# Kernel tuning notes

Hardware: AMD Instinct MI355X
Metric: run time of the kernel (lower is better)

## Reference

```python
import jax, jax.numpy as jnp
import numpy as np
import math

B, N, CS, CZ, H, HD, PQ, PV = 1, 512, 1024, 128, 12, 16, 4, 8
INF, EPS = 1e5, 1e-8


def _quat_to_rot(q):
    q = q / jnp.linalg.norm(q, axis=-1, keepdims=True)
    w, x, y, z = q[..., 0], q[..., 1], q[..., 2], q[..., 3]
    R = jnp.stack([
        1 - 2 * (y * y + z * z), 2 * (x * y - w * z), 2 * (x * z + w * y),
        2 * (x * y + w * z), 1 - 2 * (x * x + z * z), 2 * (y * z - w * x),
        2 * (x * z - w * y), 2 * (y * z + w * x), 1 - 2 * (x * x + y * y)
    ], axis=-1)
    return R.reshape(q.shape[:-1] + (3, 3))


def _split3(x):
    # torch.split into 3 chunks along last dim, then stack on new last dim
    d = x.shape[-1] // 3
    return jnp.stack((x[..., :d], x[..., d:2 * d], x[..., 2 * d:]), axis=-1)


def setup_inputs():
    key = jax.random.key(0)
    ks = jax.random.split(key, 12)

    def lin(k, din, dout):
        kw, kb = jax.random.split(k)
        W = jax.random.normal(kw, (din, dout), jnp.float32) / np.float32(np.sqrt(din))
        b = jax.random.normal(kb, (dout,), jnp.float32) * 0.01
        return W, b

    s = jax.random.normal(ks[0], (B, N, CS), jnp.float32)
    z = jax.random.normal(ks[1], (B, N, N, CZ), jnp.float32)
    rot = _quat_to_rot(jax.random.normal(ks[2], (B, N, 4), jnp.float32))
    trans = jax.random.normal(ks[3], (B, N, 3), jnp.float32) * 10.0
    mask = jnp.ones((B, N), jnp.float32)

    Wq, bq = lin(ks[4], CS, H * HD)
    Wkv, bkv = lin(ks[5], CS, 2 * H * HD)
    Wqp, bqp = lin(ks[6], CS, H * PQ * 3)
    Wkvp, bkvp = lin(ks[7], CS, H * (PQ + PV) * 3)
    Wb, bb = lin(ks[8], CZ, H)
    head_w = jax.random.normal(ks[9], (H,), jnp.float32) * 0.5
    Wout, bout = lin(ks[10], H * (CZ + HD + PV * 4), CS)

    return dict(s=s, z=z, rot=rot, trans=trans, mask=mask,
                Wq=Wq, bq=bq, Wkv=Wkv, bkv=bkv, Wqp=Wqp, bqp=bqp,
                Wkvp=Wkvp, bkvp=bkvp, Wb=Wb, bb=bb, head_w=head_w,
                Wout=Wout, bout=bout)


def _ipa(s, z, rot, trans, mask, Wq, bq, Wkv, bkv, Wqp, bqp, Wkvp, bkvp, Wb, bb, head_w, Wout, bout):
    # scalar q, k, v : [B, N, H, HD]
    q = (s @ Wq + bq).reshape(B, N, H, HD)
    kv = (s @ Wkv + bkv).reshape(B, N, H, 2 * HD)
    k, v = kv[..., :HD], kv[..., HD:]

    # point q/k/v in global frame: p' = R p + t
    q_pts = _split3(s @ Wqp + bqp)                      # [B, N, H*PQ, 3]
    q_pts = jnp.einsum('bnij,bnpj->bnpi', rot, q_pts) + trans[:, :, None, :]
    q_pts = q_pts.reshape(B, N, H, PQ, 3)

    kv_pts = _split3(s @ Wkvp + bkvp)                   # [B, N, H*(PQ+PV), 3]
    kv_pts = jnp.einsum('bnij,bnpj->bnpi', rot, kv_pts) + trans[:, :, None, :]
    kv_pts = kv_pts.reshape(B, N, H, PQ + PV, 3)
    k_pts, v_pts = kv_pts[..., :PQ, :], kv_pts[..., PQ:, :]

    # pair bias [B, N, N, H]
    b = z @ Wb + bb

    # scalar attention logits [B, H, N, N]
    a = jnp.einsum('bihd,bjhd->bhij', q, k) * np.float32(math.sqrt(1.0 / (3 * HD)))
    a = a + np.float32(math.sqrt(1.0 / 3)) * jnp.transpose(b, (0, 3, 1, 2))

    # point-distance attention: [B, N, N, H, PQ]
    diff = q_pts[:, :, None] - k_pts[:, None]           # [B, N, N, H, PQ, 3]
    pt_att = jnp.sum(diff * diff, axis=-1)
    hw = jax.nn.softplus(head_w) * np.float32(math.sqrt(1.0 / (3 * (PQ * 9.0 / 2))))
    pt_att = jnp.sum(pt_att * hw[:, None], axis=-1) * (-0.5)   # [B, N, N, H]
    a = a + jnp.transpose(pt_att, (0, 3, 1, 2))

    square_mask = INF * (mask[:, :, None] * mask[:, None, :] - 1.0)  # [B, N, N]
    a = jax.nn.softmax(a + square_mask[:, None], axis=-1)            # [B, H, N, N]

    # scalar output [B, N, H*HD]
    o = jnp.einsum('bhij,bjhd->bihd', a, v).reshape(B, N, H * HD)

    # point output, back to local frame: R^T (p - t)
    o_pt = jnp.einsum('bhij,bjhpc->bihpc', a, v_pts)                 # [B, N, H, PV, 3]
    o_pt = jnp.einsum('bnji,bnhpj->bnhpi', rot, o_pt - trans[:, :, None, None, :])
    o_pt_norm = jnp.sqrt(jnp.sum(o_pt * o_pt, axis=-1) + EPS).reshape(B, N, H * PV)
    o_pt_r = o_pt.reshape(B, N, H * PV, 3)

    # pair output [B, N, H*CZ]
    o_pair = jnp.einsum('bhij,bijc->bihc', a, z).reshape(B, N, H * CZ)

    cat = jnp.concatenate(
        (o, o_pt_r[..., 0], o_pt_r[..., 1], o_pt_r[..., 2], o_pt_norm, o_pair), axis=-1)
    return cat @ Wout + bout


def reference(s, z, rot, trans, mask, Wq, bq, Wkv, bkv, Wqp, bqp, Wkvp, bkvp, Wb, bb, head_w, Wout, bout):
    return _ipa(s, z, rot, trans, mask, Wq, bq, Wkv, bkv, Wqp, bqp, Wkvp, bkvp, Wb, bb, head_w, Wout, bout)
```

## Files before the change

kernel.cpp:

```cpp
#include <hip/hip_runtime.h>
#include <hip/hip_bf16.h>

#define N 512
#define CS 1024
#define CZ 128
#define H 12
#define HD 16

__device__ int sniff_f32(const unsigned short* p) {
    int bad = 0;
    for (int i = 0; i < 32; ++i) {
        unsigned short u = p[i];
        int e = (u >> 7) & 0xFF;
        if (e == 0xFF || e >= 141 || (e <= 27 && (u & 0x7FFFu) != 0)) bad++;
    }
    return bad > 0;
}

__device__ __forceinline__ float ld(const void* p, int i, int f32) {
    return f32 ? ((const float*)p)[i]
               : __bfloat162float(((const __hip_bfloat16*)p)[i]);
}

__device__ __forceinline__ float bfu(unsigned short u) {
    return __bfloat162float(*(const __hip_bfloat16*)&u);
}

typedef __attribute__((ext_vector_type(8))) short bf16x8;
typedef __attribute__((ext_vector_type(4))) float f32x4;
typedef __attribute__((ext_vector_type(4))) unsigned short u16x4;
typedef __attribute__((ext_vector_type(8))) unsigned short u16x8;

#define FG_LDA 40

__device__ __forceinline__ unsigned int split_bf16(float x) {
    __hip_bfloat16 hb = __float2bfloat16(x);
    float hf = __bfloat162float(hb);
    __hip_bfloat16 lb = __float2bfloat16(x - hf);
    unsigned int h = *reinterpret_cast<unsigned short*>(&hb);
    unsigned int l = *reinterpret_cast<unsigned short*>(&lb);
    return h | (l << 16);
}

__device__ __forceinline__ void wcat_resolve(int col,
        const void* Wq, const void* Wkv, const void* Wqp, const void* Wkvp,
        const void*& W, int& cc, int& ldim) {
    if (col < 192)      { W = Wq;   cc = col;       ldim = 192; }
    else if (col < 576) { W = Wkv;  cc = col - 192; ldim = 384; }
    else if (col < 720) { W = Wqp;  cc = col - 576; ldim = 144; }
    else                { W = Wkvp; cc = col - 720; ldim = 432; }
}

__global__ void proj_gemm(const void* s,
                          const void* Wq, const void* Wkv,
                          const void* Wqp, const void* Wkvp,
                          float* rawP)
{
    __shared__ unsigned short Ah[32][FG_LDA], Al[32][FG_LDA];
    __shared__ unsigned short Bh[64][FG_LDA], Bl[64][FG_LDA];
    __shared__ int flag;
    int t = threadIdx.x;
    int bn = blockIdx.x;
    int bm = blockIdx.y;
    if (t == 0) flag = sniff_f32((const unsigned short*)s);
    __syncthreads();
    int f32 = flag;

    int w  = t >> 6, l = t & 63;
    int wm = w >> 1, wn = w & 1;
    int lr = l & 15, lq = l >> 4;

    int am = t >> 3, aq = t & 7;
    int bc = t >> 2, bq = t & 3;

    const void* Wsrc; int wcc, wld;
    wcat_resolve(bn * 64 + bc, Wq, Wkv, Wqp, Wkvp, Wsrc, wcc, wld);

    f32x4 acc0 = {0.f, 0.f, 0.f, 0.f};
    f32x4 acc1 = {0.f, 0.f, 0.f, 0.f};

    int arowbase = (bm * 32 + am) * CS;

    for (int kt = 0; kt < CS / 32; ++kt) {
        {
            int base = arowbase + kt * 32 + aq * 4;
            u16x4 hh, ll;
            #pragma unroll
            for (int e = 0; e < 4; ++e) {
                unsigned int pe = split_bf16(ld(s, base + e, f32));
                hh[e] = (unsigned short)pe; ll[e] = (unsigned short)(pe >> 16);
            }
            *(u16x4*)&Ah[am][aq * 4] = hh;
            *(u16x4*)&Al[am][aq * 4] = ll;
        }
        {
            int kbase = kt * 32 + bq * 8;
            u16x8 hh, ll;
            #pragma unroll
            for (int e = 0; e < 8; ++e) {
                unsigned int pe = split_bf16(ld(Wsrc, (kbase + e) * wld + wcc, f32));
                hh[e] = (unsigned short)pe; ll[e] = (unsigned short)(pe >> 16);
            }
            *(u16x8*)&Bh[bc][bq * 8] = hh;
            *(u16x8*)&Bl[bc][bq * 8] = ll;
        }
        __syncthreads();
        bf16x8 a_h = *(const bf16x8*)&Ah[wm * 16 + lr][lq * 8];
        bf16x8 a_l = *(const bf16x8*)&Al[wm * 16 + lr][lq * 8];
        bf16x8 b0h = *(const bf16x8*)&Bh[wn * 32 + lr][lq * 8];
        bf16x8 b0l = *(const bf16x8*)&Bl[wn * 32 + lr][lq * 8];
        bf16x8 b1h = *(const bf16x8*)&Bh[wn * 32 + 16 + lr][lq * 8];
        bf16x8 b1l = *(const bf16x8*)&Bl[wn * 32 + 16 + lr][lq * 8];
        acc0 = __builtin_amdgcn_mfma_f32_16x16x32_bf16(a_h, b0h, acc0, 0, 0, 0);
        acc0 = __builtin_amdgcn_mfma_f32_16x16x32_bf16(a_h, b0l, acc0, 0, 0, 0);
        acc0 = __builtin_amdgcn_mfma_f32_16x16x32_bf16(a_l, b0h, acc0, 0, 0, 0);
        acc1 = __builtin_amdgcn_mfma_f32_16x16x32_bf16(a_h, b1h, acc1, 0, 0, 0);
        acc1 = __builtin_amdgcn_mfma_f32_16x16x32_bf16(a_h, b1l, acc1, 0, 0, 0);
        acc1 = __builtin_amdgcn_mfma_f32_16x16x32_bf16(a_l, b1h, acc1, 0, 0, 0);
        __syncthreads();
    }

    int col0 = bn * 64 + wn * 32 + lr;
    int row0 = bm * 32 + wm * 16 + lq * 4;
    #pragma unroll
    for (int r = 0; r < 4; ++r) {
        rawP[(row0 + r) * 1152 + col0]      = acc0[r];
        rawP[(row0 + r) * 1152 + col0 + 16] = acc1[r];
    }
}

__global__ void proj_post(const float* rawP,
                          const void* bq, const void* bkv,
                          const void* bqp, const void* bkvp,
                          const void* rot, const void* trans, const void* s,
                          float* q, float* k, float* v,
                          float* qp, float* kp, float* vp)
{
    __shared__ float rawL[576];
    __shared__ float R[9], T[3];
    __shared__ int flag;
    int t = threadIdx.x;
    int i = blockIdx.x;
    if (t == 0) flag = sniff_f32((const unsigned short*)s);
    __syncthreads();
    int f32 = flag;

    {
        float val = rawP[i * 1152 + t];
        if (t < 192) q[i * 192 + t] = val + ld(bq, t, f32);
        else {
            int cc = t - 192;
            float vv = val + ld(bkv, cc, f32);
            int h = cc >> 5, t2 = cc & 31;
            if (t2 < 16) k[i * 192 + h * 16 + t2] = vv;
            else         v[i * 192 + h * 16 + (t2 - 16)] = vv;
        }
    }
    rawL[t] = rawP[i * 1152 + 576 + t]
            + (t < 144 ? ld(bqp, t, f32) : ld(bkvp, t - 144, f32));
    if (t < 9) R[t] = ld(rot, i * 9 + t, f32);
    if (t >= 16 && t < 19) T[t - 16] = ld(trans, i * 3 + (t - 16), f32);
    __syncthreads();
    if (t < 192) {
        float x, y, zc;
        if (t < 48) { x = rawL[t];        y = rawL[48 + t];   zc = rawL[96 + t]; }
        else { int pk = t - 48;
               x = rawL[144 + pk]; y = rawL[288 + pk]; zc = rawL[432 + pk]; }
        float rx = R[0]*x + R[1]*y + R[2]*zc + T[0];
        float ry = R[3]*x + R[4]*y + R[5]*zc + T[1];
        float rz = R[6]*x + R[7]*y + R[8]*zc + T[2];
        if (t < 48) {
            int h = t >> 2, pp = t & 3, b = i * 144 + h * 12 + pp * 3;
            qp[b] = rx; qp[b + 1] = ry; qp[b + 2] = rz;
        } else {
            int pk = t - 48, h = pk / 12, idx = pk % 12;
            if (idx < 4) { int b = i * 144 + h * 12 + idx * 3;
                           kp[b] = rx; kp[b + 1] = ry; kp[b + 2] = rz; }
            else         { int b = i * 288 + h * 24 + (idx - 4) * 3;
                           vp[b] = rx; vp[b + 1] = ry; vp[b + 2] = rz; }
        }
    }
}

__global__ void attn_fused(const float* q, const float* k, const float* v,
                           const float* qp, const float* kp, const float* vp,
                           const void* z, const void* Wb, const void* bb,
                           const void* head_w, const void* mask,
                           const void* rot, const void* trans, const void* s,
                           float* cat)
{
    __shared__ float attL[H * N];
    __shared__ float WbL[CZ * H];
    __shared__ float pairP[4 * H * CZ];
    __shared__ float qL[192], qpL[144];
    __shared__ float RL[9], TL[3], bbL[H], hwL[H];
    __shared__ float miS;
    __shared__ int flag;
    int t = threadIdx.x;
    int i = blockIdx.x;
    if (t == 0) flag = sniff_f32((const unsigned short*)s);
    __syncthreads();
    int f32 = flag;
    for (int idx = t; idx < CZ * H; idx += 512) WbL[idx] = ld(Wb, idx, f32);
    if (t < 192) qL[t] = q[i * 192 + t];
    else if (t < 336) qpL[t - 192] = qp[i * 144 + (t - 192)];
    else if (t < 345) RL[t - 336] = ld(rot, i * 9 + (t - 336), f32);
    else if (t < 348) TL[t - 345] = ld(trans, i * 3 + (t - 345), f32);
    else if (t < 360) bbL[t - 348] = ld(bb, t - 348, f32);
    else if (t < 372) {
        float x = ld(head_w, t - 360, f32);
        float sp = (x > 20.f) ? x : log1pf(expf(x));
        hwL[t - 360] = sp * 0.13608276348795434f;
    }
    else if (t == 372) miS = ld(mask, i, f32);
    __syncthreads();

    {
        int j = t;
        float bj[H];
        #pragma unroll
        for (int h = 0; h < H; ++h) bj[h] = bbL[h];
        int zbase = (i * N + j) * CZ;

        if (f32) {
            const float4* zp = (const float4*)((const float*)z + zbase);
            #pragma unroll 4
            for (int c4 = 0; c4 < CZ / 4; ++c4) {
                float4 zv = zp[c4];
                int c0 = c4 * 4;
                #pragma unroll
                for (int h = 0; h < H; ++h)
                    bj[h] += zv.x * WbL[(c0 + 0) * H + h]
                           + zv.y * WbL[(c0 + 1) * H + h]
                           + zv.z * WbL[(c0 + 2) * H + h]
                           + zv.w * WbL[(c0 + 3) * H + h];
            }
        } else {
            const ushort4* zp = (const ushort4*)((const unsigned short*)z + zbase);
            #pragma unroll 4
            for (int c4 = 0; c4 < CZ / 4; ++c4) {
                ushort4 u = zp[c4];
                float zx = bfu(u.x), zy = bfu(u.y), zz = bfu(u.z), zw = bfu(u.w);
                int c0 = c4 * 4;
                #pragma unroll
                for (int h = 0; h < H; ++h)
                    bj[h] += zx * WbL[(c0 + 0) * H + h]
                           + zy * WbL[(c0 + 1) * H + h]
                           + zz * WbL[(c0 + 2) * H + h]
                           + zw * WbL[(c0 + 3) * H + h];
            }
        }

        float mj = ld(mask, j, f32);
        float mterm = 100000.0f * (miS * mj - 1.0f);
        const float4* kj4  = (const float4*)&k[j * 192];
        const float4* kp4  = (const float4*)&kp[j * 144];
        #pragma unroll
        for (int h = 0; h < H; ++h) {
            float4 ka = kj4[h * 4 + 0], kb = kj4[h * 4 + 1];
            float4 kc = kj4[h * 4 + 2], kd = kj4[h * 4 + 3];
            float qk = qL[h*16+ 0]*ka.x + qL[h*16+ 1]*ka.y + qL[h*16+ 2]*ka.z + qL[h*16+ 3]*ka.w
                     + qL[h*16+ 4]*kb.x + qL[h*16+ 5]*kb.y + qL[h*16+ 6]*kb.z + qL[h*16+ 7]*kb.w
                     + qL[h*16+ 8]*kc.x + qL[h*16+ 9]*kc.y + qL[h*16+10]*kc.z + qL[h*16+11]*kc.w
                     + qL[h*16+12]*kd.x + qL[h*16+13]*kd.y + qL[h*16+14]*kd.z + qL[h*16+15]*kd.w;
            float4 p0 = kp4[h * 3 + 0], p1 = kp4[h * 3 + 1], p2 = kp4[h * 3 + 2];
            float dx0 = qpL[h*12+ 0]-p0.x, dy0 = qpL[h*12+ 1]-p0.y, dz0 = qpL[h*12+ 2]-p0.z;
            float dx1 = qpL[h*12+ 3]-p0.w, dy1 = qpL[h*12+ 4]-p1.x, dz1 = qpL[h*12+ 5]-p1.y;
            float dx2 = qpL[h*12+ 6]-p1.z, dy2 = qpL[h*12+ 7]-p1.w, dz2 = qpL[h*12+ 8]-p2.x;
            float dx3 = qpL[h*12+ 9]-p2.y, dy3 = qpL[h*12+10]-p2.z, dz3 = qpL[h*12+11]-p2.w;
            float pt = dx0*dx0 + dy0*dy0 + dz0*dz0
                     + dx1*dx1 + dy1*dy1 + dz1*dz1
                     + dx2*dx2 + dy2*dy2 + dz2*dz2
                     + dx3*dx3 + dy3*dy3 + dz3*dz3;
            attL[h * N + j] = qk * 0.14433756729740643f
                            + 0.5773502691896258f * bj[h]
                            - 0.5f * hwL[h] * pt + mterm;
        }
    }
    __syncthreads();

    {
        int w = t >> 6, l = t & 63;
        for (int h = w; h < H; h += 8) {
            float av[8];
            #pragma unroll
            for (int kk = 0; kk < 8; ++kk) av[kk] = attL[h * N + kk * 64 + l];
            float m = av[0];
            #pragma unroll
            for (int kk = 1; kk < 8; ++kk) m = fmaxf(m, av[kk]);
            for (int off = 1; off < 64; off <<= 1) m = fmaxf(m, __shfl_xor(m, off));
            float ssum = 0.f;
            #pragma unroll
            for (int kk = 0; kk < 8; ++kk) { av[kk] = __expf(av[kk] - m); ssum += av[kk]; }
            for (int off = 1; off < 64; off <<= 1) ssum += __shfl_xor(ssum, off);
            float inv = 1.0f / ssum;
            #pragma unroll
            for (int kk = 0; kk < 8; ++kk) attL[h * N + kk * 64 + l] = av[kk] * inv;
        }
    }
    __syncthreads();

    if (t < 192) {
        int h = t >> 4, d = t & 15;
        float acc = 0.f;
        for (int j = 0; j < N; ++j) acc += attL[h * N + j] * v[j * 192 + h * 16 + d];
        cat[i * 2112 + t] = acc;
    } else if (t < 288) {
        int hp = t - 192, h = hp >> 3, p = hp & 7;
        float ax = 0, ay = 0, az = 0;
        for (int j = 0; j < N; ++j) {
            float a_ = attL[h * N + j];
            int b2 = j * 288 + h * 24 + p * 3;
            ax += a_ * vp[b2]; ay += a_ * vp[b2 + 1]; az += a_ * vp[b2 + 2];
        }
        float gx = ax - TL[0], gy = ay - TL[1], gz = az - TL[2];
        float lx = RL[0]*gx + RL[3]*gy + RL[6]*gz;
        float ly = RL[1]*gx + RL[4]*gy + RL[7]*gz;
        float lz = RL[2]*gx + RL[5]*gy + RL[8]*gz;
        float nrm = sqrtf(lx*lx + ly*ly + lz*lz + 1e-8f);
        cat[i * 2112 + 192 + hp] = lx;
        cat[i * 2112 + 288 + hp] = ly;
        cat[i * 2112 + 384 + hp] = lz;
        cat[i * 2112 + 480 + hp] = nrm;
    }

    {
        int quarter = t >> 7, c = t & 127;
        float pacc[H];
        #pragma unroll
        for (int h = 0; h < H; ++h) pacc[h] = 0.f;
        int j0 = quarter * 128;
        for (int j = j0; j < j0 + 128; ++j) {
            float zc = ld(z, (i * N + j) * CZ + c, f32);
            #pragma unroll
            for (int h = 0; h < H; ++h) pacc[h] += attL[h * N + j] * zc;
        }
        #pragma unroll
        for (int h = 0; h < H; ++h) pairP[quarter * (H * CZ) + h * CZ + c] = pacc[h];
    }
    __syncthreads();
    for (int idx = t; idx < H * CZ; idx += 512)
        cat[i * 2112 + 576 + idx] =
            pairP[idx] + pairP[1536 + idx] + pairP[3072 + idx] + pairP[4608 + idx];
}

__global__ void final_gemm(const float* cat, const void* Wout, const void* bout,
                           void* out, const void* s)
{
    __shared__ unsigned short Ah[32][FG_LDA], Al[32][FG_LDA];
    __shared__ unsigned short Bh[64][FG_LDA], Bl[64][FG_LDA];
    __shared__ int flag;
    int t = threadIdx.x;
    int bn = blockIdx.x;
    int bm = blockIdx.y;
    if (t == 0) flag = sniff_f32((const unsigned short*)s);
    __syncthreads();
    int f32 = flag;

    int w  = t >> 6, l = t & 63;
    int wm = w >> 1, wn = w & 1;
    int lr = l & 15, lq = l >> 4;

    int am = t >> 3, aq = t & 7;
    int bc = t >> 2, bq = t & 3;

    f32x4 acc0 = {0.f, 0.f, 0.f, 0.f};
    f32x4 acc1 = {0.f, 0.f, 0.f, 0.f};

    const float* arow = &cat[(bm * 32 + am) * 2112];

    for (int kt = 0; kt < 2112 / 32; ++kt) {
        {
            float4 xv = *(const float4*)&arow[kt * 32 + aq * 4];
            unsigned int p0 = split_bf16(xv.x);
            unsigned int p1 = split_bf16(xv.y);
            unsigned int p2 = split_bf16(xv.z);
            unsigned int p3 = split_bf16(xv.w);
            u16x4 hh, ll;
            hh[0] = (unsigned short)p0; ll[0] = (unsigned short)(p0 >> 16);
            hh[1] = (unsigned short)p1; ll[1] = (unsigned short)(p1 >> 16);
            hh[2] = (unsigned short)p2; ll[2] = (unsigned short)(p2 >> 16);
            hh[3] = (unsigned short)p3; ll[3] = (unsigned short)(p3 >> 16);
            *(u16x4*)&Ah[am][aq * 4] = hh;
            *(u16x4*)&Al[am][aq * 4] = ll;
        }
        {
            int kbase = kt * 32 + bq * 8;
            u16x8 hh, ll;
            #pragma unroll
            for (int e = 0; e < 8; ++e) {
                float x = ld(Wout, (kbase + e) * CS + bn * 64 + bc, f32);
                unsigned int pe = split_bf16(x);
                hh[e] = (unsigned short)pe;
                ll[e] = (unsigned short)(pe >> 16);
            }
            *(u16x8*)&Bh[bc][bq * 8] = hh;
            *(u16x8*)&Bl[bc][bq * 8] = ll;
        }
        __syncthreads();
        bf16x8 a_h = *(const bf16x8*)&Ah[wm * 16 + lr][lq * 8];
        bf16x8 a_l = *(const bf16x8*)&Al[wm * 16 + lr][lq * 8];
        bf16x8 b0h = *(const bf16x8*)&Bh[wn * 32 + lr][lq * 8];
        bf16x8 b0l = *(const bf16x8*)&Bl[wn * 32 + lr][lq * 8];
        bf16x8 b1h = *(const bf16x8*)&Bh[wn * 32 + 16 + lr][lq * 8];
        bf16x8 b1l = *(const bf16x8*)&Bl[wn * 32 + 16 + lr][lq * 8];
        acc0 = __builtin_amdgcn_mfma_f32_16x16x32_bf16(a_h, b0h, acc0, 0, 0, 0);
        acc0 = __builtin_amdgcn_mfma_f32_16x16x32_bf16(a_h, b0l, acc0, 0, 0, 0);
        acc0 = __builtin_amdgcn_mfma_f32_16x16x32_bf16(a_l, b0h, acc0, 0, 0, 0);
        acc1 = __builtin_amdgcn_mfma_f32_16x16x32_bf16(a_h, b1h, acc1, 0, 0, 0);
        acc1 = __builtin_amdgcn_mfma_f32_16x16x32_bf16(a_h, b1l, acc1, 0, 0, 0);
        acc1 = __builtin_amdgcn_mfma_f32_16x16x32_bf16(a_l, b1h, acc1, 0, 0, 0);
        __syncthreads();
    }

    int col0 = bn * 64 + wn * 32 + lr;
    int row0 = bm * 32 + wm * 16 + lq * 4;
    float bv0 = ld(bout, col0, f32);
    float bv1 = ld(bout, col0 + 16, f32);
    if (f32) {
        float* o = (float*)out;
        #pragma unroll
        for (int r = 0; r < 4; ++r) {
            o[(row0 + r) * CS + col0]      = acc0[r] + bv0;
            o[(row0 + r) * CS + col0 + 16] = acc1[r] + bv1;
        }
    } else {
        __hip_bfloat16* o = (__hip_bfloat16*)out;
        #pragma unroll
        for (int r = 0; r < 4; ++r) {
            o[(row0 + r) * CS + col0]      = __float2bfloat16(acc0[r] + bv0);
            o[(row0 + r) * CS + col0 + 16] = __float2bfloat16(acc1[r] + bv1);
        }
    }
}

extern "C" void kernel_launch(void* const* d_in, const int* in_sizes, int n_in,
                              void* d_out, int out_size, void* d_ws, size_t ws_size,
                              hipStream_t stream)
{
    const void* s      = d_in[0];
    const void* z      = d_in[1];
    const void* rot    = d_in[2];
    const void* trans  = d_in[3];
    const void* mask   = d_in[4];
    const void* Wq     = d_in[5];  const void* bq   = d_in[6];
    const void* Wkv    = d_in[7];  const void* bkv  = d_in[8];
    const void* Wqp    = d_in[9];  const void* bqp  = d_in[10];
    const void* Wkvp   = d_in[11]; const void* bkvp = d_in[12];
    const void* Wb     = d_in[13]; const void* bb   = d_in[14];
    const void* head_w = d_in[15];
    const void* Wout   = d_in[16]; const void* bout = d_in[17];

    float* w   = (float*)d_ws;
    float* q   = w;
    float* k   = q  + 98304;
    float* v   = k  + 98304;
    float* qp  = v  + 98304;
    float* kp  = qp + 73728;
    float* vp  = kp + 73728;
    float* cat = vp + 147456;
    float* rawP = cat;
    (void)ws_size; (void)in_sizes; (void)n_in; (void)out_size;

    proj_gemm <<<dim3(18, 16), 256, 0, stream>>>(s, Wq, Wkv, Wqp, Wkvp, rawP);
    proj_post <<<512, 576, 0, stream>>>(rawP, bq, bkv, bqp, bkvp, rot, trans, s,
                                        q, k, v, qp, kp, vp);
    attn_fused<<<512, 512, 0, stream>>>(q, k, v, qp, kp, vp, z, Wb, bb, head_w, mask,
                                        rot, trans, s, cat);
    final_gemm<<<dim3(16, 16), 256, 0, stream>>>(cat, Wout, bout, d_out, s);
}
```

Baseline: 510.6 us.

## Stage z tiles in shared memory for pair bias and transpose k layouts

The pair-bias projection now loads z in coalesced 32-row tiles into shared memory, and 12 of every 16 threads each compute one head's bias, instead of each thread streaming its own strided z row. k and kp are written transposed by the projection post-kernel, so the per-j loads in the attention logits are coalesced across threads. The pair-output loop is specialized per dtype, and the old partial-sum buffer is reused as the z staging buffer. The cost is extra barriers per tile and a quarter of threads idle during the bias step.

```diff
diff --git a/kernel.cpp b/kernel.cpp
--- a/kernel.cpp
+++ b/kernel.cpp
@@ -133,8 +133,8 @@
                           const void* bq, const void* bkv,
                           const void* bqp, const void* bkvp,
                           const void* rot, const void* trans, const void* s,
-                          float* q, float* k, float* v,
-                          float* qp, float* kp, float* vp)
+                          float* q, float* kT, float* v,
+                          float* qp, float* kpT, float* vp)
 {
     __shared__ float rawL[576];
     __shared__ float R[9], T[3];
@@ -152,7 +152,7 @@
             int cc = t - 192;
             float vv = val + ld(bkv, cc, f32);
             int h = cc >> 5, t2 = cc & 31;
-            if (t2 < 16) k[i * 192 + h * 16 + t2] = vv;
+            if (t2 < 16) kT[(h * 16 + t2) * 512 + i] = vv;
             else         v[i * 192 + h * 16 + (t2 - 16)] = vv;
         }
     }
@@ -174,16 +174,21 @@
             qp[b] = rx; qp[b + 1] = ry; qp[b + 2] = rz;
         } else {
             int pk = t - 48, h = pk / 12, idx = pk % 12;
-            if (idx < 4) { int b = i * 144 + h * 12 + idx * 3;
-                           kp[b] = rx; kp[b + 1] = ry; kp[b + 2] = rz; }
-            else         { int b = i * 288 + h * 24 + (idx - 4) * 3;
-                           vp[b] = rx; vp[b + 1] = ry; vp[b + 2] = rz; }
-        }
-    }
-}
-
-__global__ void attn_fused(const float* q, const float* k, const float* v,
-                           const float* qp, const float* kp, const float* vp,
+            if (idx < 4) {
+                int row = h * 12 + idx * 3;
+                kpT[(row + 0) * 512 + i] = rx;
+                kpT[(row + 1) * 512 + i] = ry;
+                kpT[(row + 2) * 512 + i] = rz;
+            } else {
+                int b = i * 288 + h * 24 + (idx - 4) * 3;
+                vp[b] = rx; vp[b + 1] = ry; vp[b + 2] = rz;
+            }
+        }
+    }
+}
+
+__global__ void attn_fused(const float* q, const float* kT, const float* v,
+                           const float* qp, const float* kpT, const float* vp,
                            const void* z, const void* Wb, const void* bb,
                            const void* head_w, const void* mask,
                            const void* rot, const void* trans, const void* s,
@@ -191,7 +196,7 @@
 {
     __shared__ float attL[H * N];
     __shared__ float WbL[CZ * H];
-    __shared__ float pairP[4 * H * CZ];
+    __shared__ float U[6144];
     __shared__ float qL[192], qpL[144];
     __shared__ float RL[9], TL[3], bbL[H], hwL[H];
     __shared__ float miS;
@@ -216,62 +221,63 @@
     __syncthreads();
 
     {
+        int jl = t >> 4, hs = t & 15;
+        for (int jt = 0; jt < 16; ++jt) {
+            __syncthreads();
+            if (f32) {
+                const float* zrow = (const float*)z + (i * N + jt * 32) * CZ;
+                #pragma unroll
+                for (int r = 0; r < 2; ++r) {
+                    int flat = (t + 512 * r) * 4;
+                    int row = flat >> 7, col = flat & 127;
+                    float4 vz = *(const float4*)&zrow[flat];
+                    *(float4*)&U[row * 132 + col] = vz;
+                }
+            } else {
+                const unsigned short* zrow =
+                    (const unsigned short*)z + (i * N + jt * 32) * CZ;
+                int flat = t * 8;
+                int row = flat >> 7, col = flat & 127;
+                u16x8 uv = *(const u16x8*)&zrow[flat];
+                float4 lo = {bfu(uv[0]), bfu(uv[1]), bfu(uv[2]), bfu(uv[3])};
+                float4 hi = {bfu(uv[4]), bfu(uv[5]), bfu(uv[6]), bfu(uv[7])};
+                *(float4*)&U[row * 132 + col] = lo;
+                *(float4*)&U[row * 132 + col + 4] = hi;
+            }
+            __syncthreads();
+            if (hs < H) {
+                float acc = bbL[hs];
+                #pragma unroll 8
+                for (int c = 0; c < CZ; ++c)
+                    acc += U[jl * 132 + c] * WbL[c * H + hs];
+                attL[hs * N + jt * 32 + jl] = acc;
+            }
+        }
+    }
+    __syncthreads();
+
+    {
         int j = t;
+        float mj = ld(mask, j, f32);
+        float mterm = 100000.0f * (miS * mj - 1.0f);
+        const float* kTj  = kT + j;
+        const float* kpTj = kpT + j;
         float bj[H];
         #pragma unroll
-        for (int h = 0; h < H; ++h) bj[h] = bbL[h];
-        int zbase = (i * N + j) * CZ;
-
-        if (f32) {
-            const float4* zp = (const float4*)((const float*)z + zbase);
-            #pragma unroll 4
-            for (int c4 = 0; c4 < CZ / 4; ++c4) {
-                float4 zv = zp[c4];
-                int c0 = c4 * 4;
-                #pragma unroll
-                for (int h = 0; h < H; ++h)
-                    bj[h] += zv.x * WbL[(c0 + 0) * H + h]
-                           + zv.y * WbL[(c0 + 1) * H + h]
-                           + zv.z * WbL[(c0 + 2) * H + h]
-                           + zv.w * WbL[(c0 + 3) * H + h];
-            }
-        } else {
-            const ushort4* zp = (const ushort4*)((const unsigned short*)z + zbase);
-            #pragma unroll 4
-            for (int c4 = 0; c4 < CZ / 4; ++c4) {
-                ushort4 u = zp[c4];
-                float zx = bfu(u.x), zy = bfu(u.y), zz = bfu(u.z), zw = bfu(u.w);
-                int c0 = c4 * 4;
-                #pragma unroll
-                for (int h = 0; h < H; ++h)
-                    bj[h] += zx * WbL[(c0 + 0) * H + h]
-                           + zy * WbL[(c0 + 1) * H + h]
-                           + zz * WbL[(c0 + 2) * H + h]
-                           + zw * WbL[(c0 + 3) * H + h];
-            }
-        }
-
-        float mj = ld(mask, j, f32);
-        float mterm = 100000.0f * (miS * mj - 1.0f);
-        const float4* kj4  = (const float4*)&k[j * 192];
-        const float4* kp4  = (const float4*)&kp[j * 144];
-        #pragma unroll
+        for (int h = 0; h < H; ++h) bj[h] = attL[h * N + j];
         for (int h = 0; h < H; ++h) {
-            float4 ka = kj4[h * 4 + 0], kb = kj4[h * 4 + 1];
-            float4 kc = kj4[h * 4 + 2], kd = kj4[h * 4 + 3];
-            float qk = qL[h*16+ 0]*ka.x + qL[h*16+ 1]*ka.y + qL[h*16+ 2]*ka.z + qL[h*16+ 3]*ka.w
-                     + qL[h*16+ 4]*kb.x + qL[h*16+ 5]*kb.y + qL[h*16+ 6]*kb.z + qL[h*16+ 7]*kb.w
-                     + qL[h*16+ 8]*kc.x + qL[h*16+ 9]*kc.y + qL[h*16+10]*kc.z + qL[h*16+11]*kc.w
-                     + qL[h*16+12]*kd.x + qL[h*16+13]*kd.y + qL[h*16+14]*kd.z + qL[h*16+15]*kd.w;
-            float4 p0 = kp4[h * 3 + 0], p1 = kp4[h * 3 + 1], p2 = kp4[h * 3 + 2];
-            float dx0 = qpL[h*12+ 0]-p0.x, dy0 = qpL[h*12+ 1]-p0.y, dz0 = qpL[h*12+ 2]-p0.z;
-            float dx1 = qpL[h*12+ 3]-p0.w, dy1 = qpL[h*12+ 4]-p1.x, dz1 = qpL[h*12+ 5]-p1.y;
-            float dx2 = qpL[h*12+ 6]-p1.z, dy2 = qpL[h*12+ 7]-p1.w, dz2 = qpL[h*12+ 8]-p2.x;
-            float dx3 = qpL[h*12+ 9]-p2.y, dy3 = qpL[h*12+10]-p2.z, dz3 = qpL[h*12+11]-p2.w;
-            float pt = dx0*dx0 + dy0*dy0 + dz0*dz0
-                     + dx1*dx1 + dy1*dy1 + dz1*dz1
-                     + dx2*dx2 + dy2*dy2 + dz2*dz2
-                     + dx3*dx3 + dy3*dy3 + dz3*dz3;
+            float qk = 0.f;
+            #pragma unroll
+            for (int d = 0; d < 16; ++d)
+                qk += qL[h * 16 + d] * kTj[(h * 16 + d) * 512];
+            float pt = 0.f;
+            #pragma unroll
+            for (int p = 0; p < 4; ++p) {
+                float dx = qpL[h*12 + p*3 + 0] - kpTj[(h*12 + p*3 + 0) * 512];
+                float dy = qpL[h*12 + p*3 + 1] - kpTj[(h*12 + p*3 + 1) * 512];
+                float dz = qpL[h*12 + p*3 + 2] - kpTj[(h*12 + p*3 + 2) * 512];
+                pt += dx * dx + dy * dy + dz * dz;
+            }
             attL[h * N + j] = qk * 0.14433756729740643f
                             + 0.5773502691896258f * bj[h]
                             - 0.5f * hwL[h] * pt + mterm;
@@ -330,18 +336,30 @@
         #pragma unroll
         for (int h = 0; h < H; ++h) pacc[h] = 0.f;
         int j0 = quarter * 128;
-        for (int j = j0; j < j0 + 128; ++j) {
-            float zc = ld(z, (i * N + j) * CZ + c, f32);
-            #pragma unroll
-            for (int h = 0; h < H; ++h) pacc[h] += attL[h * N + j] * zc;
-        }
+        if (f32) {
+            const float* zp = (const float*)z + (i * N + j0) * CZ + c;
+            for (int j = 0; j < 128; ++j) {
+                float zc = zp[j * CZ];
+                #pragma unroll
+                for (int h = 0; h < H; ++h) pacc[h] += attL[h * N + j0 + j] * zc;
+            }
+        } else {
+            const unsigned short* zp =
+                (const unsigned short*)z + (i * N + j0) * CZ + c;
+            for (int j = 0; j < 128; ++j) {
+                float zc = bfu(zp[j * CZ]);
+                #pragma unroll
+                for (int h = 0; h < H; ++h) pacc[h] += attL[h * N + j0 + j] * zc;
+            }
+        }
+        __syncthreads();
         #pragma unroll
-        for (int h = 0; h < H; ++h) pairP[quarter * (H * CZ) + h * CZ + c] = pacc[h];
+        for (int h = 0; h < H; ++h) U[quarter * (H * CZ) + h * CZ + c] = pacc[h];
     }
     __syncthreads();
     for (int idx = t; idx < H * CZ; idx += 512)
         cat[i * 2112 + 576 + idx] =
-            pairP[idx] + pairP[1536 + idx] + pairP[3072 + idx] + pairP[4608 + idx];
+            U[idx] + U[1536 + idx] + U[3072 + idx] + U[4608 + idx];
 }
 
 __global__ void final_gemm(const float* cat, const void* Wout, const void* bout,
@@ -451,21 +469,21 @@
     const void* head_w = d_in[15];
     const void* Wout   = d_in[16]; const void* bout = d_in[17];
 
-    float* w   = (float*)d_ws;
-    float* q   = w;
-    float* k   = q  + 98304;
-    float* v   = k  + 98304;
-    float* qp  = v  + 98304;
-    float* kp  = qp + 73728;
-    float* vp  = kp + 73728;
-    float* cat = vp + 147456;
+    float* w    = (float*)d_ws;
+    float* q    = w;
+    float* kT   = q   + 98304;
+    float* v    = kT  + 98304;
+    float* qp   = v   + 98304;
+    float* kpT  = qp  + 73728;
+    float* vp   = kpT + 73728;
+    float* cat  = vp  + 147456;
     float* rawP = cat;
     (void)ws_size; (void)in_sizes; (void)n_in; (void)out_size;
 
     proj_gemm <<<dim3(18, 16), 256, 0, stream>>>(s, Wq, Wkv, Wqp, Wkvp, rawP);
     proj_post <<<512, 576, 0, stream>>>(rawP, bq, bkv, bqp, bkvp, rot, trans, s,
-                                        q, k, v, qp, kp, vp);
-    attn_fused<<<512, 512, 0, stream>>>(q, k, v, qp, kp, vp, z, Wb, bb, head_w, mask,
+                                        q, kT, v, qp, kpT, vp);
+    attn_fused<<<512, 512, 0, stream>>>(q, kT, v, qp, kpT, vp, z, Wb, bb, head_w, mask,
                                         rot, trans, s, cat);
     final_gemm<<<dim3(16, 16), 256, 0, stream>>>(cat, Wout, bout, d_out, s);
 }
```

Result: faster. 457.2 us (-10.5%).
